# Optimization experiments

Measured on AMD Instinct MI355X. Metric: run time of the kernel, lower is better.

Reference implementation:

```python
import jax, jax.numpy as jnp
import numpy as np

B, S, IN, H, O, K = 64, 256, 512, 1024, 512, 4


def setup_inputs() -> dict:
    key = jax.random.key(0)
    ks = jax.random.split(key, 8)
    s = 1.0 / np.sqrt(H)  # torch RNNCell/Linear default uniform init bound
    return {
        "x_seq": jax.random.normal(ks[0], (B, S, IN), jnp.float32),
        "y_seq": jax.random.randint(ks[1], (B, S), 0, O, dtype=jnp.int64),
        "seq_mask": jnp.ones((B, S, 1), jnp.float32),
        "forced_num_ticks": K,
        "W_ih": jax.random.uniform(ks[2], (3 * H, IN), jnp.float32, -s, s),
        "W_hh": jax.random.uniform(ks[3], (3 * H, H), jnp.float32, -s, s),
        "b_ih": jax.random.uniform(ks[4], (3 * H,), jnp.float32, -s, s),
        "b_hh": jax.random.uniform(ks[5], (3 * H,), jnp.float32, -s, s),
        "W_fc": jax.random.uniform(ks[6], (O, H), jnp.float32, -s, s),
        "b_fc": jax.random.uniform(ks[7], (O,), jnp.float32, -s, s),
    }


def gru_cell(x, h, W_ih, W_hh, b_ih, b_hh):
    # torch.nn.GRUCell math
    gi = x @ W_ih.T + b_ih  # [B, 3H]
    gh = h @ W_hh.T + b_hh  # [B, 3H]
    i_r, i_z, i_n = jnp.split(gi, 3, axis=-1)
    h_r, h_z, h_n = jnp.split(gh, 3, axis=-1)
    r = jax.nn.sigmoid(i_r + h_r)
    z = jax.nn.sigmoid(i_z + h_z)
    n = jnp.tanh(i_n + r * h_n)
    return (1.0 - z) * n + z * h


def reference(x_seq, y_seq, seq_mask, forced_num_ticks, W_ih, W_hh, b_ih, b_hh, W_fc, b_fc):
    k = int(forced_num_ticks)
    b = x_seq.shape[0]
    # With forced_num_ticks=k, the inner while-loop runs exactly k ticks per
    # timestep for every sample; the same x_t / seq_mask[:,t,:] are reused
    # for all k ticks, and hidden state persists across timesteps.
    xs = jnp.repeat(x_seq, k, axis=1).transpose(1, 0, 2)      # [S*k, B, IN]
    sms = jnp.repeat(seq_mask, k, axis=1).transpose(1, 0, 2)  # [S*k, B, 1]
    h0 = jnp.zeros((b, W_hh.shape[1]), x_seq.dtype)

    def step(h, inp):
        x_t, sm_t = inp
        h_new = gru_cell(x_t, h, W_ih, W_hh, b_ih, b_hh)
        logits_t = (h_new @ W_fc.T + b_fc) * sm_t  # mask = not_finished * sm_t (not_finished always True)
        return h_new, logits_t

    _, logits = jax.lax.scan(step, h0, (xs, sms))  # logits: [S*k, B, O]
    logits_seq = logits.transpose(1, 0, 2)         # [B, S*k, O]
    y_res = jnp.repeat(y_seq, k, axis=1)           # [B, S*k]
    ok = jnp.repeat(seq_mask[:, :, 0] != 0, k, axis=1)  # [B, S*k] bool (mask_last=True)
    return logits_seq, y_res, ok
```

## Files before the change

### kernel.cpp

```cpp
#include <hip/hip_runtime.h>
#include <hip/hip_bf16.h>

#define B_ 64
#define S_ 256
#define IN_ 512
#define H_ 1024
#define O_ 512
#define K_ 4
#define T_ (S_*K_)
#define H3_ (3*H_)

#define NC_ 8
#define CPC_ 32
#define RPC_ 8

typedef __attribute__((ext_vector_type(8))) short bf16x8;
typedef __attribute__((ext_vector_type(4))) float f32x4;
typedef __attribute__((ext_vector_type(4))) unsigned int uint32x4;
typedef unsigned short ushort_t;
typedef unsigned int uint_t;

__device__ __forceinline__ ushort_t f2b(float f) {
    union { float f; unsigned u; } v; v.f = f;
    unsigned r = v.u + 0x7FFFu + ((v.u >> 16) & 1u);
    return (ushort_t)(r >> 16);
}
__device__ __forceinline__ float b2f(ushort_t h) {
    union { unsigned u; float f; } v; v.u = ((unsigned)h) << 16; return v.f;
}

__global__ __launch_bounds__(256) void gi_gemm(const float* __restrict__ x,
                                               const float* __restrict__ Wih,
                                               const float* __restrict__ bih,
                                               ushort_t* __restrict__ gi) {
    const int NB = H3_ / 64;
    const int nb = blockIdx.x % NB;
    const int mb = blockIdx.x / NB;
    const int tid = threadIdx.x, lane = tid & 63, w = tid >> 6;
    const int wm = w >> 1, wn = w & 1;
    __shared__ ushort_t Al[64][40];
    __shared__ ushort_t Bl[64][40];
    f32x4 acc[2][2] = {};
    const int lrow = tid >> 2, lk = (tid & 3) * 8;
    for (int k0 = 0; k0 < IN_; k0 += 32) {
        const float* xs = &x[(size_t)(mb*64 + lrow)*IN_ + k0 + lk];
        const float* ws = &Wih[(size_t)(nb*64 + lrow)*IN_ + k0 + lk];
        #pragma unroll
        for (int i = 0; i < 8; ++i) Al[lrow][lk+i] = f2b(xs[i]);
        #pragma unroll
        for (int i = 0; i < 8; ++i) Bl[lrow][lk+i] = f2b(ws[i]);
        __syncthreads();
        const int fr = lane & 15, fk = (lane >> 4) * 8;
        #pragma unroll
        for (int mt = 0; mt < 2; ++mt) {
            bf16x8 a = *(const bf16x8*)&Al[wm*32 + mt*16 + fr][fk];
            #pragma unroll
            for (int nt = 0; nt < 2; ++nt) {
                bf16x8 b = *(const bf16x8*)&Bl[wn*32 + nt*16 + fr][fk];
                acc[mt][nt] = __builtin_amdgcn_mfma_f32_16x16x32_bf16(a, b, acc[mt][nt], 0, 0, 0);
            }
        }
        __syncthreads();
    }
    const int fr = lane & 15, fm = (lane >> 4) * 4;
    #pragma unroll
    for (int mt = 0; mt < 2; ++mt)
    #pragma unroll
    for (int nt = 0; nt < 2; ++nt)
    #pragma unroll
    for (int i = 0; i < 4; ++i) {
        int gm = mb*64 + wm*32 + mt*16 + fm + i;
        int gn = nb*64 + wn*32 + nt*16 + fr;
        gi[(size_t)gm*H3_ + gn] = f2b(acc[mt][nt][i] + bih[gn]);
    }
}

__global__ __launch_bounds__(256) void rec_kernel(const ushort_t* __restrict__ gi,
                                                  const float* __restrict__ Whh,
                                                  const float* __restrict__ bhh,
                                                  ushort_t* __restrict__ hstates,
                                                  ushort_t* __restrict__ xbuf,
                                                  int* __restrict__ flags) {
    const int bid = blockIdx.x;
    const int c  = bid & 7;
    const int cu = bid >> 3;
    const int tid = threadIdx.x, lane = tid & 63, w = tid >> 6;
    const int r_el = tid >> 5, jl = tid & 31;
    const int fr = lane & 15, koff8 = (lane >> 4) << 3;
    const int colbase = cu << 5;
    const int b0 = c * RPC_;

    __shared__ ushort_t wlds[48][1036];
    __shared__ float red[4][8][100];

    for (int e = tid * 4; e < 48 * 1024; e += 256 * 4) {
        int rr = e >> 10, k = e & 1023;
        int wrow = (rr < 32) ? (colbase + rr) : (H_ + colbase + (rr - 32));
        const float* src = &Whh[(size_t)wrow*H_ + k];
        #pragma unroll
        for (int i = 0; i < 4; ++i) wlds[rr][k + i] = f2b(src[i]);
    }
    bf16x8 bz1[8], bn0[8], bn1[8];
    #pragma unroll
    for (int ks = 0; ks < 8; ++ks) {
        const int kk = (w << 8) + (ks << 5) + koff8;
        const float* sz = &Whh[(size_t)(H_   + colbase + 16 + fr)*H_ + kk];
        const float* s0 = &Whh[(size_t)(2*H_ + colbase      + fr)*H_ + kk];
        const float* s1 = &Whh[(size_t)(2*H_ + colbase + 16 + fr)*H_ + kk];
        bf16x8 tz, t0, t1;
        #pragma unroll
        for (int i = 0; i < 8; ++i) {
            tz[i] = (short)f2b(sz[i]); t0[i] = (short)f2b(s0[i]); t1[i] = (short)f2b(s1[i]);
        }
        bz1[ks] = tz; bn0[ks] = t0; bn1[ks] = t1;
    }
    const float bh_r = bhh[colbase + jl];
    const float bh_z = bhh[H_ + colbase + jl];
    const float bh_n = bhh[2*H_ + colbase + jl];

    ushort_t g_r, g_z, g_n, p_r = 0, p_z = 0, p_n = 0;
    {
        size_t row = ((size_t)(b0 + r_el)*S_ + 0)*H3_ + colbase + jl;
        g_r = gi[row]; g_z = gi[row + H_]; g_n = gi[row + 2*H_];
    }
    float gir = 0.f, giz = 0.f, gin = 0.f;

    const char* xb_lane = (const char*)xbuf
        + ((size_t)c << 16)
        + (size_t)(lane & 7) * 2048
        + (w << 9)
        + ((lane >> 4) << 4);

    float h_prev = 0.f;
    int* cflags = &flags[c << 5];
    __syncthreads();

    for (int t = 0; t < T_; ++t) {
        if ((t & 3) == 0) {
            if (t > 0) { g_r = p_r; g_z = p_z; g_n = p_n; }
            gir = b2f(g_r); giz = b2f(g_z); gin = b2f(g_n);
        }

        uint32x4 f0 = {}, f1 = {}, f2 = {}, f3 = {}, f4 = {}, f5 = {}, f6 = {}, f7 = {};
        if (t > 0) {
            const char* ab = xb_lane + (((size_t)((t - 1) & 1)) << 15);
            asm volatile(
                "global_load_dwordx4 %0, %8, off sc0 sc1\n\t"
                "global_load_dwordx4 %1, %8, off offset:64 sc0 sc1\n\t"
                "global_load_dwordx4 %2, %8, off offset:128 sc0 sc1\n\t"
                "global_load_dwordx4 %3, %8, off offset:192 sc0 sc1\n\t"
                "global_load_dwordx4 %4, %8, off offset:256 sc0 sc1\n\t"
                "global_load_dwordx4 %5, %8, off offset:320 sc0 sc1\n\t"
                "global_load_dwordx4 %6, %8, off offset:384 sc0 sc1\n\t"
                "global_load_dwordx4 %7, %8, off offset:448 sc0 sc1\n\t"
                "s_waitcnt vmcnt(0)"
                : "=&v"(f0), "=&v"(f1), "=&v"(f2), "=&v"(f3),
                  "=&v"(f4), "=&v"(f5), "=&v"(f6), "=&v"(f7)
                : "v"(ab)
                : "memory");
            __builtin_amdgcn_sched_barrier(0);
        }
        bf16x8 afr[8];
        afr[0] = *(bf16x8*)&f0; afr[1] = *(bf16x8*)&f1;
        afr[2] = *(bf16x8*)&f2; afr[3] = *(bf16x8*)&f3;
        afr[4] = *(bf16x8*)&f4; afr[5] = *(bf16x8*)&f5;
        afr[6] = *(bf16x8*)&f6; afr[7] = *(bf16x8*)&f7;

        if ((t & 3) == 0) {
            int sn = (t >> 2) + 1; if (sn > S_ - 1) sn = S_ - 1;
            size_t row = ((size_t)(b0 + r_el)*S_ + sn)*H3_ + colbase + jl;
            p_r = gi[row]; p_z = gi[row + H_]; p_n = gi[row + 2*H_];
        }

        f32x4 ar0 = {}, ar1 = {}, az0 = {}, az1 = {}, an0 = {}, an1 = {};
        #pragma unroll
        for (int ks = 0; ks < 8; ++ks) {
            const int k = (w << 8) + (ks << 5) + koff8;
            bf16x8 br0 = *(const bf16x8*)&wlds[fr][k];
            bf16x8 br1 = *(const bf16x8*)&wlds[16 + fr][k];
            bf16x8 bz0 = *(const bf16x8*)&wlds[32 + fr][k];
            ar0 = __builtin_amdgcn_mfma_f32_16x16x32_bf16(afr[ks], br0, ar0, 0, 0, 0);
            ar1 = __builtin_amdgcn_mfma_f32_16x16x32_bf16(afr[ks], br1, ar1, 0, 0, 0);
            az0 = __builtin_amdgcn_mfma_f32_16x16x32_bf16(afr[ks], bz0, az0, 0, 0, 0);
            az1 = __builtin_amdgcn_mfma_f32_16x16x32_bf16(afr[ks], bz1[ks], az1, 0, 0, 0);
            an0 = __builtin_amdgcn_mfma_f32_16x16x32_bf16(afr[ks], bn0[ks], an0, 0, 0, 0);
            an1 = __builtin_amdgcn_mfma_f32_16x16x32_bf16(afr[ks], bn1[ks], an1, 0, 0, 0);
        }
        if (lane < 32) {
            const int m = (lane >> 4) << 2, n = fr;
            #pragma unroll
            for (int i = 0; i < 4; ++i) {
                red[w][m+i][n]      = ar0[i];
                red[w][m+i][16+n]   = ar1[i];
                red[w][m+i][32+n]   = az0[i];
                red[w][m+i][48+n]   = az1[i];
                red[w][m+i][64+n]   = an0[i];
                red[w][m+i][80+n]   = an1[i];
            }
        }
        __syncthreads();

        float ghr = red[0][r_el][jl]    + red[1][r_el][jl]    + red[2][r_el][jl]    + red[3][r_el][jl];
        float ghz = red[0][r_el][32+jl] + red[1][r_el][32+jl] + red[2][r_el][32+jl] + red[3][r_el][32+jl];
        float ghn = red[0][r_el][64+jl] + red[1][r_el][64+jl] + red[2][r_el][64+jl] + red[3][r_el][64+jl];
        float rr_ = 1.f / (1.f + __expf(-(gir + ghr + bh_r)));
        float zz  = 1.f / (1.f + __expf(-(giz + ghz + bh_z)));
        float nn  = tanhf(gin + rr_ * (ghn + bh_n));
        float hn  = (1.f - zz) * nn + zz * h_prev;
        h_prev = hn;
        ushort_t hb = f2b(hn);

        hstates[((size_t)(b0 + r_el)*T_ + t)*H_ + colbase + jl] = hb;
        size_t xidx = ((size_t)c << 15) + ((size_t)(t & 1) << 14) + (r_el << 10) + colbase + jl;
        __hip_atomic_store(&xbuf[xidx], hb, __ATOMIC_RELAXED, __HIP_MEMORY_SCOPE_AGENT);

        __syncthreads();

        if (w == 0) {
            if (lane == 0)
                __hip_atomic_store(&cflags[cu], t + 1, __ATOMIC_RELAXED,
                                   __HIP_MEMORY_SCOPE_AGENT);
            for (;;) {
                int v = t + 1;
                if (lane < 32)
                    v = __hip_atomic_load(&cflags[lane], __ATOMIC_RELAXED,
                                          __HIP_MEMORY_SCOPE_AGENT);
                if (__all(v >= t + 1)) break;
                __builtin_amdgcn_s_sleep(1);
            }
        }
        __syncthreads();
    }
}

__global__ __launch_bounds__(256) void logits_gemm(const ushort_t* __restrict__ hstates,
                                                   const float* __restrict__ Wfc,
                                                   const float* __restrict__ bfc,
                                                   const float* __restrict__ sm,
                                                   float* __restrict__ out) {
    const int NB = O_ / 64;
    const int nb = blockIdx.x % NB;
    const int mb = blockIdx.x / NB;
    const int tid = threadIdx.x, lane = tid & 63, w = tid >> 6;
    const int wm = w >> 1, wn = w & 1;
    __shared__ ushort_t Al[64][40];
    __shared__ ushort_t Bl[64][40];
    f32x4 acc[2][2] = {};
    const int lrow = tid >> 2, lk = (tid & 3) * 8;
    for (int k0 = 0; k0 < H_; k0 += 32) {
        uint4 va = *(const uint4*)&hstates[(size_t)(mb*64 + lrow)*H_ + k0 + lk];
        *(uint4*)&Al[lrow][lk] = va;
        const float* ws = &Wfc[(size_t)(nb*64 + lrow)*H_ + k0 + lk];
        #pragma unroll
        for (int i = 0; i < 8; ++i) Bl[lrow][lk+i] = f2b(ws[i]);
        __syncthreads();
        const int fr = lane & 15, fk = (lane >> 4) * 8;
        #pragma unroll
        for (int mt = 0; mt < 2; ++mt) {
            bf16x8 a = *(const bf16x8*)&Al[wm*32 + mt*16 + fr][fk];
            #pragma unroll
            for (int nt = 0; nt < 2; ++nt) {
                bf16x8 b = *(const bf16x8*)&Bl[wn*32 + nt*16 + fr][fk];
                acc[mt][nt] = __builtin_amdgcn_mfma_f32_16x16x32_bf16(a, b, acc[mt][nt], 0, 0, 0);
            }
        }
        __syncthreads();
    }
    const int fr = lane & 15, fm = (lane >> 4) * 4;
    #pragma unroll
    for (int mt = 0; mt < 2; ++mt)
    #pragma unroll
    for (int nt = 0; nt < 2; ++nt)
    #pragma unroll
    for (int i = 0; i < 4; ++i) {
        int R  = mb*64 + wm*32 + mt*16 + fm + i;
        int gn = nb*64 + wn*32 + nt*16 + fr;
        int b  = R >> 10, t = R & (T_ - 1);
        float mval = sm[b*S_ + (t >> 2)];
        out[(size_t)R*O_ + gn] = (acc[mt][nt][i] + bfc[gn]) * mval;
    }
}

__global__ void tail_kernel(const int* __restrict__ y, const float* __restrict__ sm,
                            float* __restrict__ yout, float* __restrict__ okout) {
    int i = blockIdx.x * 256 + threadIdx.x;
    if (i < B_ * T_) {
        int b = i >> 10, t = i & 1023, s = t >> 2;
        yout[i]  = (float)y[b*S_ + s];
        okout[i] = (sm[b*S_ + s] != 0.0f) ? 1.0f : 0.0f;
    }
}

extern "C" void kernel_launch(void* const* d_in, const int* in_sizes, int n_in,
                              void* d_out, int out_size, void* d_ws, size_t ws_size,
                              hipStream_t stream) {
    (void)in_sizes; (void)n_in; (void)out_size; (void)ws_size;
    const float* x   = (const float*)d_in[0];
    const int*   y   = (const int*)d_in[1];
    const float* sm  = (const float*)d_in[2];
    const float* Wih = (const float*)d_in[4];
    const float* Whh = (const float*)d_in[5];
    const float* bih = (const float*)d_in[6];
    const float* bhh = (const float*)d_in[7];
    const float* Wfc = (const float*)d_in[8];
    const float* bfc = (const float*)d_in[9];

    char* ws = (char*)d_ws;
    ushort_t* gi      = (ushort_t*)ws;
    ushort_t* hstates = (ushort_t*)(ws + 100663296);
    ushort_t* xbuf    = (ushort_t*)(ws + 100663296 + 134217728);
    int*      flags   = (int*)(ws + 100663296 + 134217728 + 524288);

    hipMemsetAsync(flags, 0, 4096, stream);

    hipLaunchKernelGGL(gi_gemm, dim3((B_*S_/64)*(H3_/64)), dim3(256), 0, stream,
                       x, Wih, bih, gi);

    void* args[] = { (void*)&gi, (void*)&Whh, (void*)&bhh, (void*)&hstates,
                     (void*)&xbuf, (void*)&flags };
    hipLaunchCooperativeKernel((void*)rec_kernel, dim3(NC_*CPC_), dim3(256), args, 0, stream);

    hipLaunchKernelGGL(logits_gemm, dim3((B_*T_/64)*(O_/64)), dim3(256), 0, stream,
                       hstates, Wfc, bfc, sm, (float*)d_out);

    float* yout  = (float*)d_out + (size_t)B_*T_*O_;
    float* okout = yout + (size_t)B_*T_;
    hipLaunchKernelGGL(tail_kernel, dim3(B_*T_/256), dim3(256), 0, stream,
                       y, sm, yout, okout);
}
```

Measured before the change: 3.658 ms.

## Replace block barrier with per-wave flags and double-buffered reduction

Each wave now owns a disjoint set of hidden columns (remapped r_el/jl) and publishes its own progress flag right after storing its slice of h, so the two __syncthreads around the cross-block spin wait go away. All waves poll the 128 per-cluster flags at the top of the next step with no sleep. The reduction scratch is double-buffered by step parity so only one block barrier per step remains. The hstates store and the gi prefetch move after the flag publish to keep them off the critical path. The cost is more flag traffic from all waves polling at once, and correctness now depends on the vmcnt wait ordering the xbuf stores before the flag store.

```diff
diff --git a/kernel.cpp b/kernel.cpp
--- a/kernel.cpp
+++ b/kernel.cpp
@@ -85,13 +85,14 @@
     const int c  = bid & 7;
     const int cu = bid >> 3;
     const int tid = threadIdx.x, lane = tid & 63, w = tid >> 6;
-    const int r_el = tid >> 5, jl = tid & 31;
+    const int r_el = lane >> 3;
+    const int jl   = (w << 3) + (lane & 7);
     const int fr = lane & 15, koff8 = (lane >> 4) << 3;
     const int colbase = cu << 5;
     const int b0 = c * RPC_;
 
     __shared__ ushort_t wlds[48][1036];
-    __shared__ float red[4][8][100];
+    __shared__ float red[2][4][8][100];
 
     for (int e = tid * 4; e < 48 * 1024; e += 256 * 4) {
         int rr = e >> 10, k = e & 1023;
@@ -131,11 +132,24 @@
         + (w << 9)
         + ((lane >> 4) << 4);
 
+    int* cflags = &flags[c << 7];
+    const int* pollp = &cflags[(w << 5) + (lane & 31)];
+    int* myflag = &cflags[(cu << 2) + w];
+
     float h_prev = 0.f;
-    int* cflags = &flags[c << 5];
     __syncthreads();
 
     for (int t = 0; t < T_; ++t) {
+        if (t > 0) {
+            for (;;) {
+                int v;
+                asm volatile("global_load_dword %0, %1, off sc0 sc1\n\t"
+                             "s_waitcnt vmcnt(0)"
+                             : "=&v"(v) : "v"(pollp) : "memory");
+                if (__all(v >= t)) break;
+            }
+        }
+
         if ((t & 3) == 0) {
             if (t > 0) { g_r = p_r; g_z = p_z; g_n = p_n; }
             gir = b2f(g_r); giz = b2f(g_z); gin = b2f(g_n);
@@ -166,12 +180,6 @@
         afr[4] = *(bf16x8*)&f4; afr[5] = *(bf16x8*)&f5;
         afr[6] = *(bf16x8*)&f6; afr[7] = *(bf16x8*)&f7;
 
-        if ((t & 3) == 0) {
-            int sn = (t >> 2) + 1; if (sn > S_ - 1) sn = S_ - 1;
-            size_t row = ((size_t)(b0 + r_el)*S_ + sn)*H3_ + colbase + jl;
-            p_r = gi[row]; p_z = gi[row + H_]; p_n = gi[row + 2*H_];
-        }
-
         f32x4 ar0 = {}, ar1 = {}, az0 = {}, az1 = {}, an0 = {}, an1 = {};
         #pragma unroll
         for (int ks = 0; ks < 8; ++ks) {
@@ -186,23 +194,27 @@
             an0 = __builtin_amdgcn_mfma_f32_16x16x32_bf16(afr[ks], bn0[ks], an0, 0, 0, 0);
             an1 = __builtin_amdgcn_mfma_f32_16x16x32_bf16(afr[ks], bn1[ks], an1, 0, 0, 0);
         }
-        if (lane < 32) {
-            const int m = (lane >> 4) << 2, n = fr;
-            #pragma unroll
-            for (int i = 0; i < 4; ++i) {
-                red[w][m+i][n]      = ar0[i];
-                red[w][m+i][16+n]   = ar1[i];
-                red[w][m+i][32+n]   = az0[i];
-                red[w][m+i][48+n]   = az1[i];
-                red[w][m+i][64+n]   = an0[i];
-                red[w][m+i][80+n]   = an1[i];
+        {
+            const int par = t & 1;
+            if (lane < 32) {
+                const int m = (lane >> 4) << 2, n = fr;
+                #pragma unroll
+                for (int i = 0; i < 4; ++i) {
+                    red[par][w][m+i][n]      = ar0[i];
+                    red[par][w][m+i][16+n]   = ar1[i];
+                    red[par][w][m+i][32+n]   = az0[i];
+                    red[par][w][m+i][48+n]   = az1[i];
+                    red[par][w][m+i][64+n]   = an0[i];
+                    red[par][w][m+i][80+n]   = an1[i];
+                }
             }
         }
         __syncthreads();
 
-        float ghr = red[0][r_el][jl]    + red[1][r_el][jl]    + red[2][r_el][jl]    + red[3][r_el][jl];
-        float ghz = red[0][r_el][32+jl] + red[1][r_el][32+jl] + red[2][r_el][32+jl] + red[3][r_el][32+jl];
-        float ghn = red[0][r_el][64+jl] + red[1][r_el][64+jl] + red[2][r_el][64+jl] + red[3][r_el][64+jl];
+        const int par = t & 1;
+        float ghr = red[par][0][r_el][jl]    + red[par][1][r_el][jl]    + red[par][2][r_el][jl]    + red[par][3][r_el][jl];
+        float ghz = red[par][0][r_el][32+jl] + red[par][1][r_el][32+jl] + red[par][2][r_el][32+jl] + red[par][3][r_el][32+jl];
+        float ghn = red[par][0][r_el][64+jl] + red[par][1][r_el][64+jl] + red[par][2][r_el][64+jl] + red[par][3][r_el][64+jl];
         float rr_ = 1.f / (1.f + __expf(-(gir + ghr + bh_r)));
         float zz  = 1.f / (1.f + __expf(-(giz + ghz + bh_z)));
         float nn  = tanhf(gin + rr_ * (ghn + bh_n));
@@ -210,26 +222,20 @@
         h_prev = hn;
         ushort_t hb = f2b(hn);
 
-        hstates[((size_t)(b0 + r_el)*T_ + t)*H_ + colbase + jl] = hb;
         size_t xidx = ((size_t)c << 15) + ((size_t)(t & 1) << 14) + (r_el << 10) + colbase + jl;
         __hip_atomic_store(&xbuf[xidx], hb, __ATOMIC_RELAXED, __HIP_MEMORY_SCOPE_AGENT);
 
-        __syncthreads();
-
-        if (w == 0) {
-            if (lane == 0)
-                __hip_atomic_store(&cflags[cu], t + 1, __ATOMIC_RELAXED,
-                                   __HIP_MEMORY_SCOPE_AGENT);
-            for (;;) {
-                int v = t + 1;
-                if (lane < 32)
-                    v = __hip_atomic_load(&cflags[lane], __ATOMIC_RELAXED,
-                                          __HIP_MEMORY_SCOPE_AGENT);
-                if (__all(v >= t + 1)) break;
-                __builtin_amdgcn_s_sleep(1);
-            }
-        }
-        __syncthreads();
+        asm volatile("s_waitcnt vmcnt(0)" ::: "memory");
+        if (lane == 0)
+            __hip_atomic_store(myflag, t + 1, __ATOMIC_RELAXED,
+                               __HIP_MEMORY_SCOPE_AGENT);
+
+        hstates[((size_t)(b0 + r_el)*T_ + t)*H_ + colbase + jl] = hb;
+        if ((t & 3) == 0) {
+            int sn = (t >> 2) + 1; if (sn > S_ - 1) sn = S_ - 1;
+            size_t row = ((size_t)(b0 + r_el)*S_ + sn)*H3_ + colbase + jl;
+            p_r = gi[row]; p_z = gi[row + H_]; p_n = gi[row + 2*H_];
+        }
     }
 }
 
```

Result: slower. 7.388 ms (+102.0%).
